# Kernel optimization log

Hardware: AMD Instinct MI355X
Metric: run time of the kernel (lower is better)

The kernel has to match this reference:

```python
import jax, jax.numpy as jnp
import numpy as np

B, D_IN, D_H, D_OUT, E = 4096, 1024, 4096, 1024, 8
N_ACTIVE = 5              # max(1, int(8 * 0.625))
TEMP = float(np.e)        # BoltzmannGate default temperature
N_CAMP_A = E // 2


def setup_inputs() -> dict:
    key = jax.random.key(0)
    ks = jax.random.split(key, 6)
    s_in = 1.0 / np.sqrt(D_IN)
    s_h = 1.0 / np.sqrt(D_H)
    return {
        "x": jax.random.normal(ks[0], (B, D_IN), jnp.float32),
        "gate_w": jax.random.normal(ks[1], (D_IN, E), jnp.float32) * s_in,
        "gate_b": jnp.zeros((E,), jnp.float32),
        "w1": jax.random.normal(ks[2], (E, D_IN, D_H), jnp.float32) * s_in,
        "b1": jnp.zeros((E, D_H), jnp.float32),
        "w2": jax.random.normal(ks[3], (E, D_H, D_OUT), jnp.float32) * s_h,
        "b2": jnp.zeros((E, D_OUT), jnp.float32),
        "ph_alpha": jnp.array(1.0, jnp.float32),
        "ph_beta": jnp.array(0.0, jnp.float32),
    }


def _forward(x, gate_w, gate_b, w1, b1, w2, b2, ph_alpha, ph_beta):
    # BoltzmannGate: softmax over temperature-scaled scores, top-k mask, renorm
    scores = (x @ gate_w + gate_b) / TEMP                 # [B, E]
    probs = jax.nn.softmax(scores, axis=-1)
    _, topk_idx = jax.lax.top_k(probs, N_ACTIVE)          # [B, k]
    rows = jnp.arange(x.shape[0])[:, None]
    mask = jnp.zeros_like(probs).at[rows, topk_idx].set(1.0)
    w = probs * mask
    weights = w / (w.sum(axis=-1, keepdims=True) + 1e-8)  # [B, E]

    # Dense evaluation of all experts (dropout is inference-mode identity)
    h = jax.nn.relu(jnp.einsum("bi,eih->beh", x, w1) + b1)     # [B, E, H]
    e_out = jnp.einsum("beh,eho->beo", h, w2) + b2             # [B, E, O]

    # Camp A = experts [0, E//2), Camp G = experts [E//2, E)
    out_a = jnp.einsum("be,beo->bo", weights[:, :N_CAMP_A], e_out[:, :N_CAMP_A])
    out_g = jnp.einsum("be,beo->bo", weights[:, N_CAMP_A:], e_out[:, N_CAMP_A:])

    repulsion = out_a - out_g
    # PH distance proxy computed on detached tensors in torch -> stop_gradient
    diff = jax.lax.stop_gradient(repulsion)
    l2 = jnp.linalg.norm(diff, axis=-1)                   # [B]
    var = jnp.var(diff, axis=-1)                          # population var, ddof=0
    ph_dist = l2 * (1.0 + var)
    ph_corr = jax.nn.sigmoid(ph_alpha * ph_dist + ph_beta) * 2.0  # in (0, 2)
    output = repulsion * ph_corr[:, None]
    return output, out_a, out_g


def reference(x, gate_w, gate_b, w1, b1, w2, b2, ph_alpha, ph_beta):
    return _forward(x, gate_w, gate_b, w1, b1, w2, b2, ph_alpha, ph_beta)
```

## Files before the change

kernel.cpp:

```cpp
#include <hip/hip_runtime.h>
#include <hip/hip_bf16.h>
#include <stdint.h>

typedef unsigned short u16;
typedef unsigned int u32;
typedef __attribute__((ext_vector_type(4))) float f32x4;
typedef __attribute__((ext_vector_type(4))) int i32x4;
typedef __attribute__((ext_vector_type(8))) u16 u16x8;
typedef __attribute__((ext_vector_type(8))) __bf16 bf16x8;

constexpr int BATCH = 4096, DIN = 1024, DH = 4096, DOUT = 1024, NEXP = 8;
constexpr int HS_CAP = 3072;

struct Ptr4 { float* p[4]; };

__device__ __forceinline__ u16 f2bf(float f) {
  u32 u = __float_as_uint(f);
  u += 0x7fffu + ((u >> 16) & 1u);
  return (u16)(u >> 16);
}

#define GLOAD_LDS16(gp, lp)                                                    \
  __builtin_amdgcn_global_load_lds(                                           \
      (__attribute__((address_space(1))) void*)(gp),                          \
      (__attribute__((address_space(3))) void*)(lp), 16, 0, 0)

#define BAR()                                                                  \
  { asm volatile("" ::: "memory"); __builtin_amdgcn_s_barrier();               \
    asm volatile("" ::: "memory"); }
#define VM4() asm volatile("s_waitcnt vmcnt(4)" ::: "memory")
#define VM0() asm volatile("s_waitcnt vmcnt(0)" ::: "memory")

#define STG4(q0, q1, kofs, dst)                                                \
  { GLOAD_LDS16((q0) + (kofs), (dst));                                         \
    GLOAD_LDS16((q1) + (kofs), (dst) + 4096); }

__global__ void gate_kernel(const float* __restrict__ x,
                            const float* __restrict__ gw,
                            const float* __restrict__ gb,
                            float* __restrict__ wgt) {
  const int wave = threadIdx.x >> 6, lane = threadIdx.x & 63;
  const int b = blockIdx.x * 4 + wave;
  const float* xr = x + (size_t)b * DIN;
  float acc[NEXP];
#pragma unroll
  for (int e = 0; e < NEXP; ++e) acc[e] = 0.f;
  for (int k = lane; k < DIN; k += 64) {
    const float xv = xr[k];
    const f32x4 g0 = *(const f32x4*)(gw + (size_t)k * NEXP);
    const f32x4 g1 = *(const f32x4*)(gw + (size_t)k * NEXP + 4);
    acc[0] += xv * g0[0]; acc[1] += xv * g0[1];
    acc[2] += xv * g0[2]; acc[3] += xv * g0[3];
    acc[4] += xv * g1[0]; acc[5] += xv * g1[1];
    acc[6] += xv * g1[2]; acc[7] += xv * g1[3];
  }
#pragma unroll
  for (int off = 32; off; off >>= 1)
#pragma unroll
    for (int e = 0; e < NEXP; ++e) acc[e] += __shfl_xor(acc[e], off);
  if (lane == 0) {
    const float invT = 0.36787944117144233f;
    float s[NEXP], mx = -1e30f;
    for (int e = 0; e < NEXP; ++e) { s[e] = (acc[e] + gb[e]) * invT; mx = fmaxf(mx, s[e]); }
    float p[NEXP], sum = 0.f;
    for (int e = 0; e < NEXP; ++e) { p[e] = expf(s[e] - mx); sum += p[e]; }
    const float inv = 1.f / sum;
    for (int e = 0; e < NEXP; ++e) p[e] *= inv;
    float w[NEXP], wsum = 0.f;
    for (int e = 0; e < NEXP; ++e) {
      int cnt = 0;
      for (int j = 0; j < NEXP; ++j) cnt += (p[j] > p[e]) || (p[j] == p[e] && j < e);
      w[e] = (cnt < 5) ? p[e] : 0.f;
      wsum += w[e];
    }
    const float inv2 = 1.f / (wsum + 1e-8f);
    for (int e = 0; e < NEXP; ++e) wgt[(size_t)b * NEXP + e] = w[e] * inv2;
  }
}

__global__ void assign_kernel(const float* __restrict__ wgt,
                              int* __restrict__ cnt, u16* __restrict__ ridx) {
  const int b = blockIdx.x * 256 + threadIdx.x;
#pragma unroll
  for (int e = 0; e < NEXP; ++e) {
    if (wgt[(size_t)b * NEXP + e] != 0.f) {
      const int pos = atomicAdd(&cnt[e], 1);
      if (pos < BATCH) ridx[e * BATCH + pos] = (u16)b;
    }
  }
}

__global__ void gather_cvt(const float* __restrict__ x,
                           const int* __restrict__ cnt,
                           const u16* __restrict__ ridx,
                           u16* __restrict__ Xe) {
  const int e = blockIdx.y, p = blockIdx.x;
  int c = cnt[e]; c = c < HS_CAP ? c : HS_CAP;
  if (p >= c) return;
  const int row = ridx[e * BATCH + p];
  const float* s = x + (size_t)row * DIN;
  u16* d = Xe + ((size_t)e * HS_CAP + p) * DIN;
  const int t = threadIdx.x;
  const f32x4 a = *(const f32x4*)(s + t * 8);
  const f32x4 b = *(const f32x4*)(s + t * 8 + 4);
  u16x8 o;
  o[0] = f2bf(a[0]); o[1] = f2bf(a[1]); o[2] = f2bf(a[2]); o[3] = f2bf(a[3]);
  o[4] = f2bf(b[0]); o[5] = f2bf(b[1]); o[6] = f2bf(b[2]); o[7] = f2bf(b[3]);
  *(u16x8*)(d + t * 8) = o;
}

__global__ void transpose_cvt(const float* __restrict__ src, u16* __restrict__ dst,
                              int C, int ldd, size_t src_slice,
                              size_t dst_hi, size_t dst_lo) {
  __shared__ float ts[64][65];
  const int z = blockIdx.z;
  const float* s = src + (size_t)z * src_slice;
  u16* d = dst + (size_t)(z >> 2) * dst_hi + (size_t)(z & 3) * dst_lo;
  const int c0 = blockIdx.x * 64, r0 = blockIdx.y * 64;
  const int t = threadIdx.x;
  const int lr = t >> 4, lc = (t & 15) * 4;
#pragma unroll
  for (int i = 0; i < 4; ++i) {
    const f32x4 v = *(const f32x4*)(s + (size_t)(r0 + i * 16 + lr) * C + c0 + lc);
    ts[i * 16 + lr][lc] = v[0];
    ts[i * 16 + lr][lc + 1] = v[1];
    ts[i * 16 + lr][lc + 2] = v[2];
    ts[i * 16 + lr][lc + 3] = v[3];
  }
  __syncthreads();
  const int cc = t >> 3, r8 = (t & 7) * 8;
#pragma unroll
  for (int pass = 0; pass < 2; ++pass) {
    const int c = cc + pass * 32;
    u16x8 o;
#pragma unroll
    for (int j = 0; j < 8; ++j) o[j] = f2bf(ts[r8 + j][c]);
    *(u16x8*)(d + (size_t)(c0 + c) * ldd + r0 + r8) = o;
  }
}

__device__ __forceinline__ void rdB4(i32x4 rB[2][2], const char* base, int wc,
                                     int roff, int NH) {
#pragma unroll
  for (int n = 0; n < 2; ++n)
#pragma unroll
    for (int kk = 0; kk < 2; ++kk)
      rB[n][kk] = *(const i32x4*)(base + (((wc * 4 + NH * 2 + n) * 2 + kk) << 10) + roff);
}
template <int MH>
__device__ __forceinline__ void rdA8(i32x4 rA[4][2], const char* base, int wr, int roff) {
#pragma unroll
  for (int m = 0; m < 4; ++m)
#pragma unroll
    for (int kk = 0; kk < 2; ++kk)
      rA[m][kk] = *(const i32x4*)(base + (((wr * 8 + MH * 4 + m) * 2 + kk) << 10) + roff);
}
template <int MH, int NH>
__device__ __forceinline__ void mm16(f32x4 acc[8][4], const i32x4 rA[4][2],
                                     const i32x4 rB[2][2]) {
  __builtin_amdgcn_s_setprio(1);
#pragma unroll
  for (int m = 0; m < 4; ++m)
#pragma unroll
    for (int n = 0; n < 2; ++n)
#pragma unroll
      for (int kk = 0; kk < 2; ++kk)
        acc[MH * 4 + m][NH * 2 + n] = __builtin_amdgcn_mfma_f32_16x16x32_bf16(
            __builtin_bit_cast(bf16x8, rA[m][kk]),
            __builtin_bit_cast(bf16x8, rB[n][kk]),
            acc[MH * 4 + m][NH * 2 + n], 0, 0, 0);
  __builtin_amdgcn_s_setprio(0);
}

template <int EPI>
__global__ __launch_bounds__(512, 2) void gemm256(
    const u16* __restrict__ A0, int lda,
    const u16* __restrict__ Bt0, int ldb, int K,
    u16* __restrict__ dstH0, Ptr4 parts,
    const float* __restrict__ wgt, const float* __restrict__ bias0,
    const int* __restrict__ cnt, const u16* __restrict__ ridx, int camp,
    int NM, int NN) {
  __shared__ __align__(16) u16 sA[2][16384];
  __shared__ __align__(16) u16 sB[2][16384];

  const int tid = threadIdx.x;
  const int w = tid >> 6, lane = tid & 63;
  const int l15 = lane & 15, lh = lane >> 4;
  const int wr = w >> 2, wc = w & 3;

  const int total = gridDim.x;
  const int cpx = total >> 3;
  const int id = blockIdx.x;
  const int wk = (id & 7) * cpx + (id >> 3);
  const int m = wk % NM;
  const int n = (wk / NM) % NN;
  const int z = wk / (NM * NN);
  const int bM = m * 256, bN = n * 256;

  const int expert = camp * 4 + z;
  int count = cnt[expert];
  count = count < HS_CAP ? count : HS_CAP;
  if (bM >= count) return;
  const int eoff = expert * BATCH;

  const u16* A;
  const u16* Bt;
  const float* bias = bias0;
  u16* dstH = dstH0;
  if (EPI == 0) {
    A = A0 + (size_t)expert * HS_CAP * lda;
    Bt = Bt0 + (size_t)expert * DH * DIN;
    bias = bias0 + (size_t)expert * DH;
    dstH = dstH0 + (size_t)z * HS_CAP * DH;
  } else {
    A = A0 + (size_t)z * HS_CAP * lda;
    Bt = Bt0 + (size_t)z * DH;
  }

  const int lp = lane ^ ((lane & 32) >> 4);
  const int grow = (w >> 1) * 16 + (lp >> 2);
  const int gcol = (w & 1) * 32 + (lp & 3) * 8;

  const u16* qA0 = A + (size_t)(bM + grow) * lda + gcol;
  const u16* qA1 = qA0 + (size_t)64 * lda;
  const u16* qA2 = qA0 + (size_t)128 * lda;
  const u16* qA3 = qA0 + (size_t)192 * lda;
  const u16* qB0 = Bt + (size_t)(bN + grow) * ldb + gcol;
  const u16* qB1 = qB0 + (size_t)64 * ldb;
  const u16* qB2 = qB0 + (size_t)128 * ldb;
  const u16* qB3 = qB0 + (size_t)192 * ldb;

  u16* dA0 = &sA[0][w * 512];
  u16* dA1 = &sA[1][w * 512];
  u16* dB0 = &sB[0][w * 512];
  u16* dB1 = &sB[1][w * 512];

  const int roff = l15 * 64 + ((lh * 16) ^ ((l15 & 8) << 2));
  const char* cA0 = (const char*)&sA[0][0];
  const char* cA1 = (const char*)&sA[1][0];
  const char* cB0 = (const char*)&sB[0][0];
  const char* cB1 = (const char*)&sB[1][0];

  const int NT = K >> 6;
  f32x4 acc[8][4] = {};
  i32x4 rA[4][2], rB0[2][2], rB1[2][2];

  STG4(qB0, qB1, 0, dB0);
  STG4(qB2, qB3, 0, dB0 + 8192);
  STG4(qA0, qA1, 0, dA0);
  STG4(qA2, qA3, 0, dA0 + 8192);
  STG4(qB0, qB1, 64, dB1);
  STG4(qB2, qB3, 64, dB1 + 8192);
  VM4();
  BAR();

#define TILE(T, CA, CB_, DA_OT, DB_CB)                                         \
  {                                                                            \
    const int t_ = (T);                                                        \
    const bool g1 = (t_ + 1) < NT, g2 = (t_ + 2) < NT;                         \
    const int kA = (t_ + 1) * 64, kB = (t_ + 2) * 64;                          \
                                                                      \
    rdA8<0>(rA, CA, wr, roff);                                                 \
    rdB4(rB0, CB_, wc, roff, 0);                                               \
    if (g1) STG4(qA0, qA1, kA, DA_OT);                                         \
    BAR();                                                                     \
    mm16<0, 0>(acc, rA, rB0);                                                  \
    BAR();                                                                     \
                                                                      \
    rdB4(rB1, CB_, wc, roff, 1);                                               \
    if (g1) STG4(qA2, qA3, kA, DA_OT + 8192);                                  \
    BAR();                                                                     \
    mm16<0, 1>(acc, rA, rB1);                                                  \
    BAR();                                                                     \
                       \
    rdA8<1>(rA, CA, wr, roff);                                                 \
    if (g2) STG4(qB0, qB1, kB, DB_CB);                                         \
    BAR();                                                                     \
    mm16<1, 1>(acc, rA, rB1);                                                  \
    BAR();                                                                     \
                                                                      \
    if (g2) {                                                                  \
      STG4(qB2, qB3, kB, DB_CB + 8192);                                        \
      BAR();                                                                   \
      mm16<1, 0>(acc, rA, rB0);                                                \
      VM4();                                                                   \
    } else {                                                                   \
      BAR();                                                                   \
      mm16<1, 0>(acc, rA, rB0);                                                \
      VM0();                                                                   \
    }                                                                          \
    BAR();                                                                     \
  }

  for (int t = 0; t < NT; t += 2) {
    TILE(t, cA0, cB0, dA1, dB0);
    TILE(t + 1, cA1, cB1, dA0, dB1);
  }
#undef TILE

  if (EPI == 0) {
#pragma unroll
    for (int m2 = 0; m2 < 8; ++m2)
#pragma unroll
      for (int r = 0; r < 4; ++r) {
        const int pos = bM + wr * 128 + m2 * 16 + lh * 4 + r;
        if (pos >= count) continue;
        const int orow = ridx[eoff + pos];
        const float wsc = wgt[(size_t)orow * NEXP + expert];
#pragma unroll
        for (int nn = 0; nn < 4; ++nn) {
          const int col = bN + wc * 64 + nn * 16 + l15;
          float v = acc[m2][nn][r] + bias[col];
          v = fmaxf(v, 0.0f) * wsc;
          dstH[(size_t)pos * DH + col] = f2bf(v);
        }
      }
  } else {
    float* __restrict__ P = parts.p[z];
#pragma unroll
    for (int m2 = 0; m2 < 8; ++m2)
#pragma unroll
      for (int r = 0; r < 4; ++r) {
        const int pos = bM + wr * 128 + m2 * 16 + lh * 4 + r;
        if (pos >= count) continue;
        const int orow = ridx[eoff + pos];
#pragma unroll
        for (int nn = 0; nn < 4; ++nn) {
          const int col = bN + wc * 64 + nn * 16 + l15;
          P[(size_t)orow * DOUT + col] = acc[m2][nn][r];
        }
      }
  }
}

__global__ void reduce_kernel(float* __restrict__ dst,
                              const float* __restrict__ p0, const float* __restrict__ p1,
                              const float* __restrict__ p2, const float* __restrict__ p3,
                              const float* __restrict__ wgt,
                              const float* __restrict__ b2c, int camp) {
  const int b = blockIdx.x, t = threadIdx.x;
  const f32x4 wv = *(const f32x4*)(wgt + (size_t)b * NEXP + camp * 4);
  const size_t ro = (size_t)b * DOUT;
#pragma unroll
  for (int j = 0; j < 4; ++j) {
    const int i = j * 256 + t;
    float acc = wv[0] * b2c[i] + wv[1] * b2c[DOUT + i] +
                wv[2] * b2c[2 * DOUT + i] + wv[3] * b2c[3 * DOUT + i];
    acc += (wv[0] != 0.f) ? p0[ro + i] : 0.f;
    acc += (wv[1] != 0.f) ? p1[ro + i] : 0.f;
    acc += (wv[2] != 0.f) ? p2[ro + i] : 0.f;
    acc += (wv[3] != 0.f) ? p3[ro + i] : 0.f;
    dst[ro + i] = acc;
  }
}

__global__ void final_kernel(float* __restrict__ out,
                             const float* __restrict__ alpha,
                             const float* __restrict__ beta) {
  const int b = blockIdx.x, t = threadIdx.x;
  const float* pa = out + (size_t)BATCH * DOUT + (size_t)b * DOUT;
  const float* pg = out + (size_t)2 * BATCH * DOUT + (size_t)b * DOUT;
  float* po = out + (size_t)b * DOUT;
  float d[4], s1 = 0.f, s2 = 0.f;
#pragma unroll
  for (int j = 0; j < 4; ++j) {
    const int i = j * 256 + t;
    d[j] = pa[i] - pg[i];
    s1 += d[j];
    s2 += d[j] * d[j];
  }
#pragma unroll
  for (int off = 32; off; off >>= 1) {
    s1 += __shfl_xor(s1, off);
    s2 += __shfl_xor(s2, off);
  }
  __shared__ float r1[4], r2[4];
  if ((t & 63) == 0) { r1[t >> 6] = s1; r2[t >> 6] = s2; }
  __syncthreads();
  s1 = r1[0] + r1[1] + r1[2] + r1[3];
  s2 = r2[0] + r2[1] + r2[2] + r2[3];
  const float mean = s1 * (1.f / DOUT);
  const float var = s2 * (1.f / DOUT) - mean * mean;
  const float dist = sqrtf(s2) * (1.f + var);
  const float zz = alpha[0] * dist + beta[0];
  const float corr = 2.f / (1.f + expf(-zz));
#pragma unroll
  for (int j = 0; j < 4; ++j) po[j * 256 + t] = d[j] * corr;
}

extern "C" void kernel_launch(void* const* d_in, const int* in_sizes, int n_in,
                              void* d_out, int out_size, void* d_ws, size_t ws_size,
                              hipStream_t stream) {
  const float* x   = (const float*)d_in[0];
  const float* gw  = (const float*)d_in[1];
  const float* gb  = (const float*)d_in[2];
  const float* w1  = (const float*)d_in[3];
  const float* b1  = (const float*)d_in[4];
  const float* w2  = (const float*)d_in[5];
  const float* b2  = (const float*)d_in[6];
  const float* pha = (const float*)d_in[7];
  const float* phb = (const float*)d_in[8];
  float* out = (float*)d_out;
  float* out_a = out + (size_t)BATCH * DOUT;
  float* out_g = out + (size_t)2 * BATCH * DOUT;

  char* ws = (char*)d_ws;
  float* wgt = (float*)ws;
  int* cnt   = (int*)(ws + 131072);
  u16* ridx  = (u16*)(ws + 135168);
  u16* Xe    = (u16*)(ws + 262144);
  u16* w1t   = (u16*)(ws + 50593792);
  u16* w2t1  = w1t;
  u16* w2t0  = (u16*)(ws + 117702656);
  float* P0  = (float*)(ws + 151257088);
  float* P1  = (float*)(ws + 168034304);
  u16* Hs    = (u16*)(ws + 184811520);

  gate_kernel<<<BATCH / 4, 256, 0, stream>>>(x, gw, gb, wgt);
  hipMemsetAsync(cnt, 0, NEXP * sizeof(int), stream);
  assign_kernel<<<BATCH / 256, 256, 0, stream>>>(wgt, cnt, ridx);
  gather_cvt<<<dim3(HS_CAP, NEXP), 128, 0, stream>>>(x, cnt, ridx, Xe);
  transpose_cvt<<<dim3(DH / 64, DIN / 64, NEXP), 256, 0, stream>>>(
      w1, w1t, DH, DIN, (size_t)DIN * DH, (size_t)4 * DH * DIN, (size_t)DH * DIN);
  transpose_cvt<<<dim3(DOUT / 64, DH / 64, 4), 256, 0, stream>>>(
      w2, w2t0, DOUT, 4 * DH, (size_t)DH * DOUT, 0, (size_t)DH);

  Ptr4 parts0 = {{out_a, out, out_g, P0}};
  Ptr4 parts1 = {{out_g, out, P0, P1}};

  constexpr int NM1 = HS_CAP / 256, NN1 = DH / 256;
  constexpr int NM2 = HS_CAP / 256, NN2 = DOUT / 256;
  const int g1total = NM1 * NN1 * 4;
  const int g2total = NM2 * NN2 * 4;

  gemm256<0><<<g1total, 512, 0, stream>>>(
      Xe, DIN, w1t, DIN, DIN, Hs, parts0, wgt, b1, cnt, ridx, 0, NM1, NN1);
  transpose_cvt<<<dim3(DOUT / 64, DH / 64, 4), 256, 0, stream>>>(
      w2 + (size_t)4 * DH * DOUT, w2t1, DOUT, 4 * DH, (size_t)DH * DOUT, 0, (size_t)DH);
  gemm256<2><<<g2total, 512, 0, stream>>>(
      Hs, DH, w2t0, 4 * DH, DH, nullptr, parts0, nullptr, nullptr, cnt, ridx, 0, NM2, NN2);
  reduce_kernel<<<BATCH, 256, 0, stream>>>(out_a, out_a, out, out_g, P0,
                                           wgt, b2, 0);
  gemm256<0><<<g1total, 512, 0, stream>>>(
      Xe, DIN, w1t, DIN, DIN, Hs, parts1, wgt, b1, cnt, ridx, 1, NM1, NN1);
  gemm256<2><<<g2total, 512, 0, stream>>>(
      Hs, DH, w2t1, 4 * DH, DH, nullptr, parts1, nullptr, nullptr, cnt, ridx, 1, NM2, NN2);
  reduce_kernel<<<BATCH, 256, 0, stream>>>(out_g, out_g, out, P0, P1,
                                           wgt, b2 + (size_t)4 * DOUT, 1);

  final_kernel<<<BATCH, 256, 0, stream>>>(out, pha, phb);
}
```

Measured before the change: 678.4 us.

## Merge both camps' first GEMM into one launch and shrink per-expert row capacity

```diff
diff --git a/kernel.cpp b/kernel.cpp
--- a/kernel.cpp
+++ b/kernel.cpp
@@ -10,7 +10,7 @@
 typedef __attribute__((ext_vector_type(8))) __bf16 bf16x8;
 
 constexpr int BATCH = 4096, DIN = 1024, DH = 4096, DOUT = 1024, NEXP = 8;
-constexpr int HS_CAP = 3072;
+constexpr int HS_CAP = 2816;
 
 struct Ptr4 { float* p[4]; };
 
@@ -188,8 +188,7 @@
   const int l15 = lane & 15, lh = lane >> 4;
   const int wr = w >> 2, wc = w & 3;
 
-  const int total = gridDim.x;
-  const int cpx = total >> 3;
+  const int cpx = (int)gridDim.x >> 3;
   const int id = blockIdx.x;
   const int wk = (id & 7) * cpx + (id >> 3);
   const int m = wk % NM;
@@ -409,12 +408,19 @@
   int* cnt   = (int*)(ws + 131072);
   u16* ridx  = (u16*)(ws + 135168);
   u16* Xe    = (u16*)(ws + 262144);
-  u16* w1t   = (u16*)(ws + 50593792);
-  u16* w2t1  = w1t;
-  u16* w2t0  = (u16*)(ws + 117702656);
-  float* P0  = (float*)(ws + 151257088);
-  float* P1  = (float*)(ws + 168034304);
-  u16* Hs    = (u16*)(ws + 184811520);
+  constexpr size_t XE_BYTES  = (size_t)NEXP * HS_CAP * DIN * 2;
+  constexpr size_t W1T_BYTES = (size_t)NEXP * DH * DIN * 2;
+  constexpr size_t W2T_BYTES = (size_t)DOUT * 4 * DH * 2;
+  constexpr size_t P_BYTES   = (size_t)BATCH * DOUT * 4;
+  constexpr size_t HS_E      = (size_t)HS_CAP * DH * 2;
+  const size_t w1t_off = 262144 + XE_BYTES;
+  u16* w1t = (u16*)(ws + w1t_off);
+
+  const size_t merged_need = w1t_off + W1T_BYTES + 2 * P_BYTES + 8 * HS_E;
+  const bool merged = (ws_size >= merged_need);
+
+  constexpr int NM = HS_CAP / 256;
+  constexpr int NN1 = DH / 256, NN2 = DOUT / 256;
 
   gate_kernel<<<BATCH / 4, 256, 0, stream>>>(x, gw, gb, wgt);
   hipMemsetAsync(cnt, 0, NEXP * sizeof(int), stream);
@@ -422,31 +428,56 @@
   gather_cvt<<<dim3(HS_CAP, NEXP), 128, 0, stream>>>(x, cnt, ridx, Xe);
   transpose_cvt<<<dim3(DH / 64, DIN / 64, NEXP), 256, 0, stream>>>(
       w1, w1t, DH, DIN, (size_t)DIN * DH, (size_t)4 * DH * DIN, (size_t)DH * DIN);
-  transpose_cvt<<<dim3(DOUT / 64, DH / 64, 4), 256, 0, stream>>>(
-      w2, w2t0, DOUT, 4 * DH, (size_t)DH * DOUT, 0, (size_t)DH);
-
-  Ptr4 parts0 = {{out_a, out, out_g, P0}};
-  Ptr4 parts1 = {{out_g, out, P0, P1}};
-
-  constexpr int NM1 = HS_CAP / 256, NN1 = DH / 256;
-  constexpr int NM2 = HS_CAP / 256, NN2 = DOUT / 256;
-  const int g1total = NM1 * NN1 * 4;
-  const int g2total = NM2 * NN2 * 4;
-
-  gemm256<0><<<g1total, 512, 0, stream>>>(
-      Xe, DIN, w1t, DIN, DIN, Hs, parts0, wgt, b1, cnt, ridx, 0, NM1, NN1);
-  transpose_cvt<<<dim3(DOUT / 64, DH / 64, 4), 256, 0, stream>>>(
-      w2 + (size_t)4 * DH * DOUT, w2t1, DOUT, 4 * DH, (size_t)DH * DOUT, 0, (size_t)DH);
-  gemm256<2><<<g2total, 512, 0, stream>>>(
-      Hs, DH, w2t0, 4 * DH, DH, nullptr, parts0, nullptr, nullptr, cnt, ridx, 0, NM2, NN2);
-  reduce_kernel<<<BATCH, 256, 0, stream>>>(out_a, out_a, out, out_g, P0,
-                                           wgt, b2, 0);
-  gemm256<0><<<g1total, 512, 0, stream>>>(
-      Xe, DIN, w1t, DIN, DIN, Hs, parts1, wgt, b1, cnt, ridx, 1, NM1, NN1);
-  gemm256<2><<<g2total, 512, 0, stream>>>(
-      Hs, DH, w2t1, 4 * DH, DH, nullptr, parts1, nullptr, nullptr, cnt, ridx, 1, NM2, NN2);
-  reduce_kernel<<<BATCH, 256, 0, stream>>>(out_g, out_g, out, P0, P1,
-                                           wgt, b2 + (size_t)4 * DOUT, 1);
+
+  if (merged) {
+    float* P0 = (float*)(ws + w1t_off + W1T_BYTES);
+    float* P1 = (float*)(ws + w1t_off + W1T_BYTES + P_BYTES);
+    u16* Hs   = (u16*)(ws + w1t_off + W1T_BYTES + 2 * P_BYTES);
+    u16* w2t0 = w1t;
+    u16* w2t1 = (u16*)((char*)w1t + W2T_BYTES);
+    Ptr4 pc0 = {{out_a, out, out_g, P0}};
+    Ptr4 pc1 = {{out_g, out, P0, P1}};
+
+    gemm256<0><<<NM * NN1 * 8, 512, 0, stream>>>(
+        Xe, DIN, w1t, DIN, DIN, Hs, pc0, wgt, b1, cnt, ridx, 0, NM, NN1);
+    transpose_cvt<<<dim3(DOUT / 64, DH / 64, 4), 256, 0, stream>>>(
+        w2, w2t0, DOUT, 4 * DH, (size_t)DH * DOUT, 0, (size_t)DH);
+    transpose_cvt<<<dim3(DOUT / 64, DH / 64, 4), 256, 0, stream>>>(
+        w2 + (size_t)4 * DH * DOUT, w2t1, DOUT, 4 * DH, (size_t)DH * DOUT, 0, (size_t)DH);
+
+    gemm256<2><<<NM * NN2 * 4, 512, 0, stream>>>(
+        Hs, DH, w2t0, 4 * DH, DH, nullptr, pc0, nullptr, nullptr, cnt, ridx, 0, NM, NN2);
+    reduce_kernel<<<BATCH, 256, 0, stream>>>(out_a, out_a, out, out_g, P0, wgt, b2, 0);
+    gemm256<2><<<NM * NN2 * 4, 512, 0, stream>>>(
+        Hs + (size_t)4 * HS_CAP * DH, DH, w2t1, 4 * DH, DH, nullptr, pc1,
+        nullptr, nullptr, cnt, ridx, 1, NM, NN2);
+    reduce_kernel<<<BATCH, 256, 0, stream>>>(out_g, out_g, out, P0, P1, wgt,
+                                             b2 + (size_t)4 * DOUT, 1);
+  } else {
+    u16* w2t1 = w1t;
+    u16* w2t0 = (u16*)(ws + w1t_off + W1T_BYTES);
+    float* P0 = (float*)(ws + w1t_off + W1T_BYTES + W2T_BYTES);
+    float* P1 = (float*)(ws + w1t_off + W1T_BYTES + W2T_BYTES + P_BYTES);
+    u16* Hs   = (u16*)(ws + w1t_off + W1T_BYTES + W2T_BYTES + 2 * P_BYTES);
+    Ptr4 pc0 = {{out_a, out, out_g, P0}};
+    Ptr4 pc1 = {{out_g, out, P0, P1}};
+
+    transpose_cvt<<<dim3(DOUT / 64, DH / 64, 4), 256, 0, stream>>>(
+        w2, w2t0, DOUT, 4 * DH, (size_t)DH * DOUT, 0, (size_t)DH);
+    gemm256<0><<<NM * NN1 * 4, 512, 0, stream>>>(
+        Xe, DIN, w1t, DIN, DIN, Hs, pc0, wgt, b1, cnt, ridx, 0, NM, NN1);
+    transpose_cvt<<<dim3(DOUT / 64, DH / 64, 4), 256, 0, stream>>>(
+        w2 + (size_t)4 * DH * DOUT, w2t1, DOUT, 4 * DH, (size_t)DH * DOUT, 0, (size_t)DH);
+    gemm256<2><<<NM * NN2 * 4, 512, 0, stream>>>(
+        Hs, DH, w2t0, 4 * DH, DH, nullptr, pc0, nullptr, nullptr, cnt, ridx, 0, NM, NN2);
+    reduce_kernel<<<BATCH, 256, 0, stream>>>(out_a, out_a, out, out_g, P0, wgt, b2, 0);
+    gemm256<0><<<NM * NN1 * 4, 512, 0, stream>>>(
+        Xe, DIN, w1t, DIN, DIN, Hs, pc1, wgt, b1, cnt, ridx, 1, NM, NN1);
+    gemm256<2><<<NM * NN2 * 4, 512, 0, stream>>>(
+        Hs, DH, w2t1, 4 * DH, DH, nullptr, pc1, nullptr, nullptr, cnt, ridx, 1, NM, NN2);
+    reduce_kernel<<<BATCH, 256, 0, stream>>>(out_g, out_g, out, P0, P1, wgt,
+                                             b2 + (size_t)4 * DOUT, 1);
+  }
 
   final_kernel<<<BATCH, 256, 0, stream>>>(out, pha, phb);
 }
```

Result: no change. 683.0 us (+0.7%).
